# Kernel tuning notes

Hardware: AMD Instinct MI355X
Metric: run time of the kernel (lower is better)

Reference implementation:

```python
import jax, jax.numpy as jnp
import numpy as np

B, C, T = 1024, 64, 275
S = 10            # number of subjects
EMB = 184         # encoder embedding dim
PROJ = 1024       # projector dim
LN_EPS = 1e-5


def setup_inputs() -> dict:
    key = jax.random.key(0)
    ks = jax.random.split(key, 12)
    sc = lambda *shape: 1.0 / np.sqrt(shape[-1] if len(shape) > 1 else 1.0)
    return {
        "eeg": jax.random.normal(ks[0], (B, C, T), dtype=jnp.float32),
        "subject_ids": jax.random.randint(ks[1], (B,), 0, S, dtype=jnp.int64),
        # per-subject Linear(T, T): y = x @ W.T + b
        "subj_W": jax.random.normal(ks[2], (S, T, T), dtype=jnp.float32) / np.sqrt(T),
        "subj_b": jax.random.normal(ks[3], (S, T), dtype=jnp.float32) * 0.02,
        # encoder stub: flatten (C*T) -> Linear -> EMB
        "enc_W": jax.random.normal(ks[4], (C * T, EMB), dtype=jnp.float32) / np.sqrt(C * T),
        "enc_b": jnp.zeros((EMB,), dtype=jnp.float32),
        # projector: Linear(EMB, PROJ) -> ResidualAdd(GELU -> Linear(PROJ, PROJ)) -> LayerNorm
        "W1": jax.random.normal(ks[5], (EMB, PROJ), dtype=jnp.float32) / np.sqrt(EMB),
        "b1": jnp.zeros((PROJ,), dtype=jnp.float32),
        "W2": jax.random.normal(ks[6], (PROJ, PROJ), dtype=jnp.float32) / np.sqrt(PROJ),
        "b2": jnp.zeros((PROJ,), dtype=jnp.float32),
        "gamma": jnp.ones((PROJ,), dtype=jnp.float32),
        "beta": jnp.zeros((PROJ,), dtype=jnp.float32),
    }


def reference(eeg, subject_ids, subj_W, subj_b, enc_W, enc_b, W1, b1, W2, b2, gamma, beta):
    # --- subject-wise alignment: grouped gather -> linear -> scatter ---
    # Vectorized form of the per-subject loop: each row b uses weight subj_W[sid[b]].
    Wg = subj_W[subject_ids]              # [B, T, T]
    bg = subj_b[subject_ids]              # [B, T]
    # torch Linear: y = x @ W.T + b  ->  y[b,c,u] = sum_t eeg[b,c,t] * Wg[b,u,t]
    x = jnp.einsum("bct,but->bcu", eeg, Wg) + bg[:, None, :]   # [B, C, T]

    # --- encoder stub (SpatioTemporalCNN placeholder): flatten + linear ---
    h = x.reshape(x.shape[0], -1) @ enc_W + enc_b              # [B, EMB]

    # --- MLPProjector ---
    h = h @ W1 + b1                                            # [B, PROJ]
    r = jax.nn.gelu(h, approximate=False) @ W2 + b2            # dropout is identity at eval
    h = h + r
    # LayerNorm over last dim
    mu = jnp.mean(h, axis=-1, keepdims=True)
    var = jnp.mean(jnp.square(h - mu), axis=-1, keepdims=True)
    out = (h - mu) * jax.lax.rsqrt(var + LN_EPS) * gamma + beta
    return out
```

## Files before the change

kernel.cpp:

```cpp
#include <hip/hip_runtime.h>
#include <hip/hip_bf16.h>
#include <math.h>

#define B_N    1024
#define C_N    64
#define T_N    275
#define S_N    10
#define EMB_N  184
#define PROJ_N 1024
#define CT_N   (C_N * T_N)
#define TP     288
#define KP2    (C_N * TP)
#define EMBP   192
#define KZ2    16
#define KC2    (KP2 / KZ2)
#define KZ5    2
#define GMAX   264

#define SEC_W   0
#define SEC_E   810
#define SEC_1   1002
#define SEC_2   1050
#define SEC_G   1306
#define SEC_N   1307

typedef unsigned short u16;
typedef __attribute__((ext_vector_type(8))) short short8;
typedef __attribute__((ext_vector_type(4))) short short4v;
typedef __attribute__((ext_vector_type(4))) float f32x4;

#define MFMA16(a,b,c) __builtin_amdgcn_mfma_f32_16x16x32_bf16(a, b, c, 0, 0, 0)

__device__ __forceinline__ u16 f2bf(float f) {
    __hip_bfloat16 h = __float2bfloat16(f);
    return *reinterpret_cast<u16*>(&h);
}
__device__ __forceinline__ float gelu_exact(float v) {
    return 0.5f * v * (1.0f + erff(v * 0.70710678118654752f));
}
__device__ __forceinline__ void gload16(const void* g, void* lds) {
    __builtin_amdgcn_global_load_lds(
        (const __attribute__((address_space(1))) void*)g,
        (__attribute__((address_space(3))) void*)lds, 16, 0, 0);
}

__global__ __launch_bounds__(256) void p_all(
    const int* __restrict__ sid, const float* __restrict__ W,
    const float* __restrict__ encW, const float* __restrict__ W1,
    const float* __restrict__ W2, const float* __restrict__ subj_b,
    u16* __restrict__ Wb, u16* __restrict__ eT, u16* __restrict__ w1t,
    u16* __restrict__ w2t, int* __restrict__ bsq, float* __restrict__ sbp)
{
    __shared__ char smem[16640];
    const int blk = blockIdx.x;
    const int tid = threadIdx.x;

    if (blk < SEC_E) {
        int idx4 = blk * 256 + tid;
        if (idx4 >= S_N * TP * TP / 4) return;
        int o = idx4 * 4;
        int row = o / TP, t = o - row * TP;
        int s = row / TP, u = row - s * TP;
        short4v pk;
        #pragma unroll
        for (int e = 0; e < 4; ++e) {
            float v = (u < T_N && t + e < T_N)
                ? W[((size_t)s * T_N + u) * T_N + t + e] : 0.f;
            pk[e] = (short)f2bf(v);
        }
        *reinterpret_cast<short4v*>(Wb + o) = pk;
        return;
    }
    if (blk < SEC_1) {
        float (*tile)[65] = (float(*)[65])smem;
        int local = blk - SEC_E;
        const int c = local / 3;
        const int n0 = (local % 3) * 64;
        for (int u0 = 0; u0 < TP; u0 += 64) {
            int wlen = (TP - u0 < 64) ? (TP - u0) : 64;
            __syncthreads();
            for (int l = tid; l < 4096; l += 256) {
                int i = l >> 6, j = l & 63;
                int u = u0 + i, n = n0 + j;
                float v = 0.f;
                if (u < T_N && n < EMB_N)
                    v = encW[((size_t)c * T_N + u) * EMB_N + n];
                tile[i][j] = v;
            }
            __syncthreads();
            for (int l = tid; l < 4096; l += 256) {
                int j = l >> 6, i = l & 63;
                if (i < wlen)
                    eT[(size_t)(n0 + j) * KP2 + (size_t)c * TP + u0 + i] =
                        f2bf(tile[i][j]);
            }
        }
        return;
    }
    if (blk < SEC_2) {
        float (*tile)[65] = (float(*)[65])smem;
        int local = blk - SEC_1;
        const int k0 = (local % 3) * 64, n0 = (local / 3) * 64;
        for (int l = tid; l < 4096; l += 256) {
            int i = l >> 6, j = l & 63;
            float v = (k0 + i < EMB_N) ? W1[(size_t)(k0 + i) * PROJ_N + n0 + j] : 0.f;
            tile[i][j] = v;
        }
        __syncthreads();
        for (int l = tid; l < 4096; l += 256) {
            int j = l >> 6, i = l & 63;
            w1t[(size_t)(n0 + j) * EMBP + k0 + i] = f2bf(tile[i][j]);
        }
        return;
    }
    if (blk < SEC_G) {
        float (*tile)[65] = (float(*)[65])smem;
        int local = blk - SEC_2;
        const int k0 = (local % 16) * 64, n0 = (local / 16) * 64;
        for (int l = tid; l < 4096; l += 256) {
            int i = l >> 6, j = l & 63;
            tile[i][j] = W2[(size_t)(k0 + i) * PROJ_N + n0 + j];
        }
        __syncthreads();
        for (int l = tid; l < 4096; l += 256) {
            int j = l >> 6, i = l & 63;
            w2t[(size_t)(n0 + j) * PROJ_N + k0 + i] = f2bf(tile[i][j]);
        }
        return;
    }
    {
        for (int i = tid; i < S_N * TP; i += 256) {
            int s = i / TP, u = i - s * TP;
            sbp[i] = (u < T_N) ? subj_b[s * T_N + u] : 0.f;
        }
        int* sgrp = (int*)smem;
        int* C    = (int*)(smem + 4096);
        int* tot  = (int*)(smem + 4096 + 640);
        for (int i = tid; i < 1024; i += 256) sgrp[i] = sid[i];
        for (int i = tid; i < 4 * GMAX; i += 256) bsq[i] = -1;
        __syncthreads();
        const int w4 = tid >> 6, lane = tid & 63;
        #pragma unroll
        for (int j = 0; j < 4; ++j) {
            int chunk = w4 * 4 + j;
            int sb = sgrp[chunk * 64 + lane];
            int myc = 0;
            for (int s = 0; s < S_N; ++s) {
                unsigned long long m = __ballot(sb == s);
                if (lane == s) myc = (int)__popcll(m);
            }
            if (lane < S_N) C[chunk * S_N + lane] = myc;
        }
        __syncthreads();
        if (tid < S_N) {
            int a = 0;
            for (int w2 = 0; w2 < 16; ++w2) a += C[w2 * S_N + tid];
            tot[tid] = a;
        }
        __syncthreads();
        #pragma unroll
        for (int rep = 0; rep < 4; ++rep) {
            int b = tid + rep * 256;
            int s = sgrp[b];
            int off = 0;
            for (int s2 = 0; s2 < S_N; ++s2)
                if (s2 < s) off += (tot[s2] + 3) & ~3;
            int chunk = b >> 6;
            int rank = 0;
            for (int w2 = 0; w2 < 16; ++w2)
                if (w2 < chunk) rank += C[w2 * S_N + s];
            for (int i = chunk * 64; i < b; ++i) rank += (sgrp[i] == s) ? 1 : 0;
            bsq[off + rank] = b;
        }
    }
}

__global__ __launch_bounds__(512) void k1h(
    const float* __restrict__ eeg, const int* __restrict__ sid,
    const u16* __restrict__ Wb, const float* __restrict__ sbp,
    const int* __restrict__ bsq, u16* __restrict__ xb)
{
    __shared__ __align__(16) u16 Ws[2][TP * 32];
    __shared__ __align__(16) u16 Es[2][128 * 40];
    const int g = blockIdx.x;
    const int b0 = bsq[g * 4];
    if (b0 < 0) return;
    const int ch = blockIdx.y;
    const int s = sid[b0];
    const int tid = threadIdx.x;
    const int w = tid >> 6, lane = tid & 63;
    const int bi = w >> 1, uh = w & 1;
    const int lrow = lane & 15, lk = lane >> 4;
    const int b = bsq[g * 4 + bi];
    const u16* Wr = Wb + (size_t)s * TP * TP;

    const int srow = tid >> 2;
    const int quarter = tid & 3;
    const int bt = srow >> 5, cl = srow & 31;
    int bstage = bsq[g * 4 + bt]; if (bstage < 0) bstage = b0;
    const float* esrc = eeg + (size_t)bstage * CT_N + (ch * 32 + cl) * T_N;

    #define K1_WSTAGE(st, ks)                                                  \
        for (int l = tid; l < TP * 4; l += 512) {                              \
            int u_ = l >> 2, q_ = l & 3;                                       \
            gload16(Wr + (size_t)u_ * TP + (ks) * 32 + ((q_ ^ ((u_ >> 1) & 3)) << 3), \
                    &Ws[st][l * 8]);                                           \
        }
    #define K1_ELOAD(ks, v)                                                    \
        {   int t0_ = (ks) * 32 + quarter * 8;                                 \
            if ((ks) < 8) {                                                    \
                _Pragma("unroll")                                              \
                for (int e = 0; e < 8; ++e) v[e] = esrc[t0_ + e];              \
            } else {                                                           \
                _Pragma("unroll")                                              \
                for (int e = 0; e < 8; ++e)                                    \
                    v[e] = (t0_ + e < T_N) ? esrc[t0_ + e] : 0.f;              \
            }                                                                  \
        }
    #define K1_EWRITE(st, v)                                                   \
        {   short8 pk_;                                                        \
            _Pragma("unroll")                                                  \
            for (int e = 0; e < 8; ++e) pk_[e] = (short)f2bf(v[e]);            \
            *reinterpret_cast<short8*>(&Es[st][srow * 40 + quarter * 8]) = pk_;\
        }

    f32x4 acc[9][2] = {};
    float ev[8], evn[8];

    K1_WSTAGE(0, 0);
    K1_ELOAD(0, ev);
    K1_EWRITE(0, ev);
    __syncthreads();

    for (int ks = 0; ks < 9; ++ks) {
        const int st = ks & 1;
        if (ks < 8) {
            K1_WSTAGE(st ^ 1, ks + 1);
            K1_ELOAD(ks + 1, evn);
        }
        short8 ef[2];
        #pragma unroll
        for (int cf = 0; cf < 2; ++cf)
            ef[cf] = *reinterpret_cast<const short8*>(
                &Es[st][(bi * 32 + cf * 16 + lrow) * 40 + lk * 8]);
        #pragma unroll
        for (int uf = 0; uf < 9; ++uf) {
            int u = uh * 144 + uf * 16 + lrow;
            int chunk = u * 4 + (lk ^ ((u >> 1) & 3));
            short8 av = *reinterpret_cast<const short8*>(&Ws[st][chunk * 8]);
            acc[uf][0] = MFMA16(av, ef[0], acc[uf][0]);
            acc[uf][1] = MFMA16(av, ef[1], acc[uf][1]);
        }
        if (ks < 8) K1_EWRITE(st ^ 1, evn);
        __syncthreads();
    }

    if (b < 0) return;
    u16* xrow = xb + (size_t)b * KP2 + (size_t)(ch * 32) * TP;
    #pragma unroll
    for (int uf = 0; uf < 9; ++uf) {
        int ub = uh * 144 + uf * 16 + 4 * lk;
        float4 b4 = *reinterpret_cast<const float4*>(sbp + s * TP + ub);
        float bias[4] = { b4.x, b4.y, b4.z, b4.w };
        #pragma unroll
        for (int cf = 0; cf < 2; ++cf) {
            int c = cf * 16 + lrow;
            short4v pk;
            #pragma unroll
            for (int r = 0; r < 4; ++r)
                pk[r] = (ub + r < T_N) ? (short)f2bf(acc[uf][cf][r] + bias[r])
                                       : (short)0;
            *reinterpret_cast<short4v*>(xrow + (size_t)c * TP + ub) = pk;
        }
    }
    #undef K1_WSTAGE
    #undef K1_ELOAD
    #undef K1_EWRITE
}

__global__ __launch_bounds__(256) void k2_mfma(
    const u16* __restrict__ xb, const u16* __restrict__ eT,
    float* __restrict__ part)
{
    __shared__ __align__(16) u16 Ab[2][64 * 64];
    const int m0 = blockIdx.x * 64;
    const int kz = blockIdx.y;
    const int kbase = kz * KC2;
    const int tid = threadIdx.x;
    const int w = tid >> 6, lane = tid & 63;
    const int lrow = lane & 15, lk = lane >> 4;

    #define K2_STAGE(st, step)                                                 \
        _Pragma("unroll")                                                      \
        for (int p = 0; p < 2; ++p) {                                          \
            int l = tid + p * 256;                                             \
            int r_ = l >> 3, q_ = l & 7;                                       \
            gload16(xb + (size_t)(m0 + r_) * KP2 + kbase + (step) * 64 +       \
                        ((q_ ^ (r_ & 7)) << 3),                                \
                    &Ab[st][l * 8]);                                           \
        }
    #define K2_BLOAD(step, dst)                                                \
        _Pragma("unroll")                                                      \
        for (int ct = 0; ct < 3; ++ct)                                         \
            _Pragma("unroll")                                                  \
            for (int ki = 0; ki < 2; ++ki)                                     \
                dst[ct][ki] = *reinterpret_cast<const short8*>(                \
                    eT + (size_t)(48 * w + 16 * ct + lrow) * KP2 + kbase +     \
                    (step) * 64 + ki * 32 + 8 * lk);

    f32x4 acc[4][3] = {};
    short8 bf[3][2], bn[3][2];

    K2_STAGE(0, 0);
    K2_BLOAD(0, bf);
    __syncthreads();

    for (int step = 0; step < 18; ++step) {
        const int st = step & 1;
        if (step < 17) {
            K2_STAGE(st ^ 1, step + 1);
            K2_BLOAD(step + 1, bn);
        }
        #pragma unroll
        for (int ki = 0; ki < 2; ++ki)
            #pragma unroll
            for (int rt = 0; rt < 4; ++rt) {
                int m = 16 * rt + lrow;
                int chunk = m * 8 + ((4 * ki + lk) ^ (m & 7));
                short8 af = *reinterpret_cast<const short8*>(&Ab[st][chunk * 8]);
                #pragma unroll
                for (int ct = 0; ct < 3; ++ct)
                    acc[rt][ct] = MFMA16(af, bf[ct][ki], acc[rt][ct]);
            }
        __syncthreads();
        #pragma unroll
        for (int ct = 0; ct < 3; ++ct)
            #pragma unroll
            for (int ki = 0; ki < 2; ++ki) bf[ct][ki] = bn[ct][ki];
    }

    #pragma unroll
    for (int rt = 0; rt < 4; ++rt)
        #pragma unroll
        for (int ct = 0; ct < 3; ++ct) {
            int n = 48 * w + 16 * ct + lrow;
            #pragma unroll
            for (int r = 0; r < 4; ++r) {
                int m = m0 + 16 * rt + 4 * lk + r;
                part[((size_t)kz * B_N + m) * EMBP + n] = acc[rt][ct][r];
            }
        }
    #undef K2_STAGE
    #undef K2_BLOAD
}

__global__ __launch_bounds__(256) void k3_reduce(
    const float* __restrict__ part, const float* __restrict__ enc_b,
    u16* __restrict__ hb)
{
    int idx = blockIdx.x * 256 + threadIdx.x;
    if (idx >= B_N * EMBP) return;
    int n = idx % EMBP;
    float s = 0.f;
    if (n < EMB_N) {
        s = enc_b[n];
        #pragma unroll
        for (int z = 0; z < KZ2; ++z)
            s += part[(size_t)z * B_N * EMBP + idx];
    }
    hb[idx] = f2bf(s);
}

__global__ __launch_bounds__(256) void k4_mfma(
    const u16* __restrict__ hb, const u16* __restrict__ w1t,
    const float* __restrict__ b1, float* __restrict__ h1, u16* __restrict__ g)
{
    __shared__ __align__(16) u16 Ab[64 * EMBP];
    __shared__ __align__(16) u16 Bb[64 * EMBP];
    const int m0 = blockIdx.x * 64, n0 = blockIdx.y * 64;
    const int tid = threadIdx.x;
    const int w = tid >> 6, lane = tid & 63;
    const int wr = w >> 1, wc = w & 1;
    const int lrow = lane & 15, lk = lane >> 4;

    #pragma unroll
    for (int i = 0; i < 6; ++i) {
        int L = tid + i * 256;
        int row = L / 24, qp = L % 24;
        int ql = qp ^ (row & 7);
        gload16(hb  + (size_t)(m0 + row) * EMBP + ql * 8, &Ab[(size_t)L * 8]);
        gload16(w1t + (size_t)(n0 + row) * EMBP + ql * 8, &Bb[(size_t)L * 8]);
    }
    __syncthreads();

    f32x4 acc[2][2] = {};
    #pragma unroll
    for (int ks = 0; ks < 6; ++ks) {
        #pragma unroll
        for (int rt = 0; rt < 2; ++rt) {
            int c = 32 * wr + 16 * rt + lrow;
            short8 af = *reinterpret_cast<const short8*>(
                &Ab[c * EMBP + (((4 * ks + lk) ^ (c & 7)) * 8)]);
            #pragma unroll
            for (int ct = 0; ct < 2; ++ct) {
                int nl = 32 * wc + 16 * ct + lrow;
                short8 bfv = *reinterpret_cast<const short8*>(
                    &Bb[nl * EMBP + (((4 * ks + lk) ^ (nl & 7)) * 8)]);
                acc[rt][ct] = MFMA16(af, bfv, acc[rt][ct]);
            }
        }
    }
    #pragma unroll
    for (int rt = 0; rt < 2; ++rt)
        #pragma unroll
        for (int ct = 0; ct < 2; ++ct) {
            int n = n0 + 32 * wc + 16 * ct + lrow;
            #pragma unroll
            for (int r = 0; r < 4; ++r) {
                int m = m0 + 32 * wr + 16 * rt + 4 * lk + r;
                float v = acc[rt][ct][r] + b1[n];
                size_t o = (size_t)m * PROJ_N + n;
                h1[o] = v;
                g[o] = f2bf(gelu_exact(v));
            }
        }
}

__global__ __launch_bounds__(256) void k5_mfma(
    const u16* __restrict__ g, const u16* __restrict__ w2t,
    float* __restrict__ part2)
{
    __shared__ __align__(16) u16 Ab[2][64 * 64];
    __shared__ __align__(16) u16 Bb[2][64 * 64];
    const int m0 = blockIdx.x * 64, n0 = blockIdx.y * 64;
    const int kz = blockIdx.z;
    const int kbase = kz * (PROJ_N / KZ5);
    const int tid = threadIdx.x;
    const int w = tid >> 6, lane = tid & 63;
    const int wr = w >> 1, wc = w & 1;
    const int lrow = lane & 15, lk = lane >> 4;

    const int r0 = tid >> 3, q0 = tid & 7;
    const int r1 = (tid + 256) >> 3;
    const u16* a0 = g + (size_t)(m0 + r0) * PROJ_N + (q0 ^ (r0 & 7)) * 8;
    const u16* a1 = g + (size_t)(m0 + r1) * PROJ_N + (q0 ^ (r1 & 7)) * 8;
    const u16* b0 = w2t + (size_t)(n0 + r0) * PROJ_N + (q0 ^ (r0 & 7)) * 8;
    const u16* b1p = w2t + (size_t)(n0 + r1) * PROJ_N + (q0 ^ (r1 & 7)) * 8;

    f32x4 acc[2][2] = {};
    int buf = 0;
    gload16(a0 + kbase, &Ab[0][(size_t)(w * 64) * 8]);
    gload16(a1 + kbase, &Ab[0][(size_t)(w * 64 + 256) * 8]);
    gload16(b0 + kbase, &Bb[0][(size_t)(w * 64) * 8]);
    gload16(b1p + kbase, &Bb[0][(size_t)(w * 64 + 256) * 8]);
    __syncthreads();

    for (int step = 0; step < 8; ++step) {
        if (step < 7) {
            int k0 = kbase + (step + 1) * 64;
            gload16(a0 + k0, &Ab[buf ^ 1][(size_t)(w * 64) * 8]);
            gload16(a1 + k0, &Ab[buf ^ 1][(size_t)(w * 64 + 256) * 8]);
            gload16(b0 + k0, &Bb[buf ^ 1][(size_t)(w * 64) * 8]);
            gload16(b1p + k0, &Bb[buf ^ 1][(size_t)(w * 64 + 256) * 8]);
        }
        #pragma unroll
        for (int ki = 0; ki < 2; ++ki) {
            #pragma unroll
            for (int rt = 0; rt < 2; ++rt) {
                int c = 32 * wr + 16 * rt + lrow;
                short8 af = *reinterpret_cast<const short8*>(
                    &Ab[buf][c * 64 + (((lk + 4 * ki) ^ (c & 7)) * 8)]);
                #pragma unroll
                for (int ct = 0; ct < 2; ++ct) {
                    int nl = 32 * wc + 16 * ct + lrow;
                    short8 bfv = *reinterpret_cast<const short8*>(
                        &Bb[buf][nl * 64 + (((lk + 4 * ki) ^ (nl & 7)) * 8)]);
                    acc[rt][ct] = MFMA16(af, bfv, acc[rt][ct]);
                }
            }
        }
        __syncthreads();
        buf ^= 1;
    }
    #pragma unroll
    for (int rt = 0; rt < 2; ++rt)
        #pragma unroll
        for (int ct = 0; ct < 2; ++ct) {
            int n = n0 + 32 * wc + 16 * ct + lrow;
            #pragma unroll
            for (int r = 0; r < 4; ++r) {
                int m = m0 + 32 * wr + 16 * rt + 4 * lk + r;
                part2[(size_t)kz * B_N * PROJ_N + (size_t)m * PROJ_N + n] = acc[rt][ct][r];
            }
        }
}

__global__ __launch_bounds__(256) void k5r_ln(
    const float* __restrict__ part2, const float* __restrict__ h1,
    const float* __restrict__ b2, const float* __restrict__ gamma,
    const float* __restrict__ beta, float* __restrict__ out)
{
    const int m = blockIdx.x;
    const int tid = threadIdx.x;
    const float4* h4 = reinterpret_cast<const float4*>(h1 + (size_t)m * PROJ_N);
    const float4* p0 = reinterpret_cast<const float4*>(part2 + (size_t)m * PROJ_N);
    const float4* p1 = reinterpret_cast<const float4*>(part2 + (size_t)(B_N + m) * PROJ_N);
    const float4* b4 = reinterpret_cast<const float4*>(b2);
    float4 va = h4[tid], vb = p0[tid], vc = p1[tid], vd = b4[tid];
    float v[4] = { va.x + vb.x + vc.x + vd.x, va.y + vb.y + vc.y + vd.y,
                   va.z + vb.z + vc.z + vd.z, va.w + vb.w + vc.w + vd.w };
    float s = 0.f, sq = 0.f;
    #pragma unroll
    for (int i = 0; i < 4; ++i) { s += v[i]; sq += v[i] * v[i]; }
    #pragma unroll
    for (int off = 32; off > 0; off >>= 1) {
        s  += __shfl_down(s, off);
        sq += __shfl_down(sq, off);
    }
    __shared__ float ss[4], ssq[4];
    int wid = tid >> 6, lane = tid & 63;
    if (lane == 0) { ss[wid] = s; ssq[wid] = sq; }
    __syncthreads();
    if (tid == 0) {
        float a = 0.f, bsum = 0.f;
        #pragma unroll
        for (int q = 0; q < 4; ++q) { a += ss[q]; bsum += ssq[q]; }
        ss[0] = a; ssq[0] = bsum;
    }
    __syncthreads();
    float mu  = ss[0] * (1.0f / PROJ_N);
    float var = ssq[0] * (1.0f / PROJ_N) - mu * mu;
    float rs  = rsqrtf(var + 1e-5f);
    const float4 g4 = reinterpret_cast<const float4*>(gamma)[tid];
    const float4 be4 = reinterpret_cast<const float4*>(beta)[tid];
    float gg[4] = { g4.x, g4.y, g4.z, g4.w };
    float bb[4] = { be4.x, be4.y, be4.z, be4.w };
    float4 o4;
    float* op = reinterpret_cast<float*>(&o4);
    #pragma unroll
    for (int i = 0; i < 4; ++i) op[i] = (v[i] - mu) * rs * gg[i] + bb[i];
    reinterpret_cast<float4*>(out + (size_t)m * PROJ_N)[tid] = o4;
}

extern "C" void kernel_launch(void* const* d_in, const int* in_sizes, int n_in,
                              void* d_out, int out_size, void* d_ws, size_t ws_size,
                              hipStream_t stream)
{
    const float* eeg    = (const float*)d_in[0];
    const int*   sid    = (const int*)  d_in[1];
    const float* subj_W = (const float*)d_in[2];
    const float* subj_b = (const float*)d_in[3];
    const float* enc_W  = (const float*)d_in[4];
    const float* enc_b  = (const float*)d_in[5];
    const float* W1     = (const float*)d_in[6];
    const float* b1     = (const float*)d_in[7];
    const float* W2     = (const float*)d_in[8];
    const float* b2     = (const float*)d_in[9];
    const float* gamma  = (const float*)d_in[10];
    const float* beta   = (const float*)d_in[11];
    float* out = (float*)d_out;

    char* w = (char*)d_ws;
    u16*   xb    = (u16*)(w);
    u16*   Wb    = (u16*)(w + 37748736);
    u16*   eT    = (u16*)(w + 39407616);
    u16*   w1t   = (u16*)(w + 46485504);
    u16*   w2t   = (u16*)(w + 46878720);
    u16*   hb    = (u16*)(w + 48975872);
    float* h1    = (float*)(w + 49369088);
    u16*   g     = (u16*)(w + 53563392);
    float* sbp   = (float*)(w + 55660544);
    int*   bsq   = (int*)(w + 55672064);
    float* part  = (float*)(w + 55676288);
    float* part2 = (float*)(w + 68259200);

    p_all<<<dim3(SEC_N), 256, 0, stream>>>(sid, subj_W, enc_W, W1, W2, subj_b,
                                           Wb, eT, w1t, w2t, bsq, sbp);
    k1h  <<<dim3(GMAX, 2), 512, 0, stream>>>(eeg, sid, Wb, sbp, bsq, xb);
    k2_mfma<<<dim3(16, KZ2), 256, 0, stream>>>(xb, eT, part);
    k3_reduce<<<dim3((B_N * EMBP + 255) / 256), 256, 0, stream>>>(part, enc_b, hb);
    k4_mfma<<<dim3(16, 16), 256, 0, stream>>>(hb, w1t, b1, h1, g);
    k5_mfma<<<dim3(16, 16, KZ5), 256, 0, stream>>>(g, w2t, part2);
    k5r_ln <<<dim3(B_N), 256, 0, stream>>>(part2, h1, b2, gamma, beta, out);
}
```

Baseline: 120.8 us.

## Preload whole EEG tile with vectorized loads and split k1 blocks in half

The subject-alignment kernel now loads the full 32-channel by 275-sample EEG slab for two batch rows into shared memory up front, using contiguous float4 loads converted to bf16. This replaces the per-K-step strided scalar loads that were double-buffered. Blocks shrink from 512 to 256 threads and the grid doubles, so each block handles two batch rows instead of four. The trade-off is more shared memory per block, no overlap between the EEG load and compute, and the subject weight slab now being staged twice as often.

```diff
diff --git a/kernel.cpp b/kernel.cpp
--- a/kernel.cpp
+++ b/kernel.cpp
@@ -16,6 +16,7 @@
 #define KC2    (KP2 / KZ2)
 #define KZ5    2
 #define GMAX   264
+#define ESTR   296
 
 #define SEC_W   0
 #define SEC_E   810
@@ -175,74 +176,66 @@
     }
 }
 
-__global__ __launch_bounds__(512) void k1h(
+__global__ __launch_bounds__(256) void k1v(
     const float* __restrict__ eeg, const int* __restrict__ sid,
     const u16* __restrict__ Wb, const float* __restrict__ sbp,
     const int* __restrict__ bsq, u16* __restrict__ xb)
 {
+    __shared__ __align__(16) u16 Es[64 * ESTR];
     __shared__ __align__(16) u16 Ws[2][TP * 32];
-    __shared__ __align__(16) u16 Es[2][128 * 40];
     const int g = blockIdx.x;
     const int b0 = bsq[g * 4];
     if (b0 < 0) return;
-    const int ch = blockIdx.y;
+    const int p = blockIdx.y >> 1, ch = blockIdx.y & 1;
     const int s = sid[b0];
     const int tid = threadIdx.x;
     const int w = tid >> 6, lane = tid & 63;
     const int bi = w >> 1, uh = w & 1;
     const int lrow = lane & 15, lk = lane >> 4;
-    const int b = bsq[g * 4 + bi];
+    const int b = bsq[g * 4 + p * 2 + bi];
     const u16* Wr = Wb + (size_t)s * TP * TP;
 
-    const int srow = tid >> 2;
-    const int quarter = tid & 3;
-    const int bt = srow >> 5, cl = srow & 31;
-    int bstage = bsq[g * 4 + bt]; if (bstage < 0) bstage = b0;
-    const float* esrc = eeg + (size_t)bstage * CT_N + (ch * 32 + cl) * T_N;
-
     #define K1_WSTAGE(st, ks)                                                  \
-        for (int l = tid; l < TP * 4; l += 512) {                              \
+        for (int l = tid; l < TP * 4; l += 256) {                              \
             int u_ = l >> 2, q_ = l & 3;                                       \
             gload16(Wr + (size_t)u_ * TP + (ks) * 32 + ((q_ ^ ((u_ >> 1) & 3)) << 3), \
                     &Ws[st][l * 8]);                                           \
         }
-    #define K1_ELOAD(ks, v)                                                    \
-        {   int t0_ = (ks) * 32 + quarter * 8;                                 \
-            if ((ks) < 8) {                                                    \
-                _Pragma("unroll")                                              \
-                for (int e = 0; e < 8; ++e) v[e] = esrc[t0_ + e];              \
-            } else {                                                           \
-                _Pragma("unroll")                                              \
-                for (int e = 0; e < 8; ++e)                                    \
-                    v[e] = (t0_ + e < T_N) ? esrc[t0_ + e] : 0.f;              \
-            }                                                                  \
-        }
-    #define K1_EWRITE(st, v)                                                   \
-        {   short8 pk_;                                                        \
-            _Pragma("unroll")                                                  \
-            for (int e = 0; e < 8; ++e) pk_[e] = (short)f2bf(v[e]);            \
-            *reinterpret_cast<short8*>(&Es[st][srow * 40 + quarter * 8]) = pk_;\
-        }
+
+    K1_WSTAGE(0, 0);
+    #pragma unroll
+    for (int reg = 0; reg < 2; ++reg) {
+        int bstage = bsq[g * 4 + p * 2 + reg]; if (bstage < 0) bstage = b0;
+        const float4* src4 = reinterpret_cast<const float4*>(
+            eeg + (size_t)bstage * CT_N + ch * 32 * T_N);
+        for (int l = tid; l < (32 * T_N) / 4; l += 256) {
+            float4 v = src4[l];
+            float vv[4] = { v.x, v.y, v.z, v.w };
+            int o = l * 4;
+            int r = o / T_N, c0 = o - r * T_N;
+            #pragma unroll
+            for (int e = 0; e < 4; ++e) {
+                int r2 = r, c2 = c0 + e;
+                if (c2 >= T_N) { r2++; c2 -= T_N; }
+                Es[(reg * 32 + r2) * ESTR + c2] = f2bf(vv[e]);
+            }
+        }
+    }
+    for (int l = tid; l < 64 * (TP - T_N); l += 256) {
+        int r = l / (TP - T_N), c = T_N + (l - r * (TP - T_N));
+        Es[r * ESTR + c] = 0;
+    }
+    __syncthreads();
 
     f32x4 acc[9][2] = {};
-    float ev[8], evn[8];
-
-    K1_WSTAGE(0, 0);
-    K1_ELOAD(0, ev);
-    K1_EWRITE(0, ev);
-    __syncthreads();
-
     for (int ks = 0; ks < 9; ++ks) {
         const int st = ks & 1;
-        if (ks < 8) {
-            K1_WSTAGE(st ^ 1, ks + 1);
-            K1_ELOAD(ks + 1, evn);
-        }
+        if (ks < 8) K1_WSTAGE(st ^ 1, ks + 1);
         short8 ef[2];
         #pragma unroll
         for (int cf = 0; cf < 2; ++cf)
             ef[cf] = *reinterpret_cast<const short8*>(
-                &Es[st][(bi * 32 + cf * 16 + lrow) * 40 + lk * 8]);
+                &Es[(bi * 32 + cf * 16 + lrow) * ESTR + ks * 32 + lk * 8]);
         #pragma unroll
         for (int uf = 0; uf < 9; ++uf) {
             int u = uh * 144 + uf * 16 + lrow;
@@ -251,7 +244,6 @@
             acc[uf][0] = MFMA16(av, ef[0], acc[uf][0]);
             acc[uf][1] = MFMA16(av, ef[1], acc[uf][1]);
         }
-        if (ks < 8) K1_EWRITE(st ^ 1, evn);
         __syncthreads();
     }
 
@@ -274,8 +266,6 @@
         }
     }
     #undef K1_WSTAGE
-    #undef K1_ELOAD
-    #undef K1_EWRITE
 }
 
 __global__ __launch_bounds__(256) void k2_mfma(
@@ -576,7 +566,7 @@
 
     p_all<<<dim3(SEC_N), 256, 0, stream>>>(sid, subj_W, enc_W, W1, W2, subj_b,
                                            Wb, eT, w1t, w2t, bsq, sbp);
-    k1h  <<<dim3(GMAX, 2), 512, 0, stream>>>(eeg, sid, Wb, sbp, bsq, xb);
+    k1v  <<<dim3(GMAX, 4), 256, 0, stream>>>(eeg, sid, Wb, sbp, bsq, xb);
     k2_mfma<<<dim3(16, KZ2), 256, 0, stream>>>(xb, eT, part);
     k3_reduce<<<dim3((B_N * EMBP + 255) / 256), 256, 0, stream>>>(part, enc_b, hb);
     k4_mfma<<<dim3(16, 16), 256, 0, stream>>>(hb, w1t, b1, h1, g);
```

Result: slower. 130.9 us (+8.4%).

## Triple-buffer subject weight tiles in k1 with counted vmcnt waits

Applied to the files above, without the earlier changes.

The per-subject alignment GEMM kernel now keeps three LDS buffers for the weight tiles and prefetches two k-steps ahead, replacing __syncthreads with raw s_barrier plus per-wave vmcnt waits so async global-to-LDS loads can stay in flight across iterations. It also raises wave priority around the MFMA block. This is meant to hide global load latency in k1, at the cost of more LDS per block (possible occupancy loss) and fragile hand-counted vmcnt values.

```diff
diff --git a/kernel.cpp b/kernel.cpp
--- a/kernel.cpp
+++ b/kernel.cpp
@@ -175,12 +175,12 @@
     }
 }
 
-__global__ __launch_bounds__(512) void k1h(
+__global__ __launch_bounds__(512) void k1p(
     const float* __restrict__ eeg, const int* __restrict__ sid,
     const u16* __restrict__ Wb, const float* __restrict__ sbp,
     const int* __restrict__ bsq, u16* __restrict__ xb)
 {
-    __shared__ __align__(16) u16 Ws[2][TP * 32];
+    __shared__ __align__(16) u16 Ws[3][TP * 32];
     __shared__ __align__(16) u16 Es[2][128 * 40];
     const int g = blockIdx.x;
     const int b0 = bsq[g * 4];
@@ -200,11 +200,11 @@
     int bstage = bsq[g * 4 + bt]; if (bstage < 0) bstage = b0;
     const float* esrc = eeg + (size_t)bstage * CT_N + (ch * 32 + cl) * T_N;
 
-    #define K1_WSTAGE(st, ks)                                                  \
+    #define K1_WSTAGE(bufi, ks)                                                \
         for (int l = tid; l < TP * 4; l += 512) {                              \
             int u_ = l >> 2, q_ = l & 3;                                       \
             gload16(Wr + (size_t)u_ * TP + (ks) * 32 + ((q_ ^ ((u_ >> 1) & 3)) << 3), \
-                    &Ws[st][l * 8]);                                           \
+                    &Ws[bufi][l * 8]);                                         \
         }
     #define K1_ELOAD(ks, v)                                                    \
         {   int t0_ = (ks) * 32 + quarter * 8;                                 \
@@ -223,36 +223,45 @@
             for (int e = 0; e < 8; ++e) pk_[e] = (short)f2bf(v[e]);            \
             *reinterpret_cast<short8*>(&Es[st][srow * 40 + quarter * 8]) = pk_;\
         }
+    #define K1_WAITN()                                                         \
+        {   if (w < 2) asm volatile("s_waitcnt vmcnt(3) lgkmcnt(0)" ::: "memory"); \
+            else       asm volatile("s_waitcnt vmcnt(2) lgkmcnt(0)" ::: "memory"); }
 
     f32x4 acc[9][2] = {};
     float ev[8], evn[8];
 
+    K1_ELOAD(0, ev);
     K1_WSTAGE(0, 0);
-    K1_ELOAD(0, ev);
+    K1_WSTAGE(1, 1);
     K1_EWRITE(0, ev);
-    __syncthreads();
+    K1_WAITN();
+    __builtin_amdgcn_s_barrier();
 
     for (int ks = 0; ks < 9; ++ks) {
-        const int st = ks & 1;
-        if (ks < 8) {
-            K1_WSTAGE(st ^ 1, ks + 1);
-            K1_ELOAD(ks + 1, evn);
-        }
+        const int wb = ks % 3, eb = ks & 1;
+        if (ks < 8) K1_ELOAD(ks + 1, evn);
+        if (ks < 7) K1_WSTAGE((ks + 2) % 3, ks + 2);
+
         short8 ef[2];
         #pragma unroll
         for (int cf = 0; cf < 2; ++cf)
             ef[cf] = *reinterpret_cast<const short8*>(
-                &Es[st][(bi * 32 + cf * 16 + lrow) * 40 + lk * 8]);
+                &Es[eb][(bi * 32 + cf * 16 + lrow) * 40 + lk * 8]);
+        __builtin_amdgcn_s_setprio(1);
         #pragma unroll
         for (int uf = 0; uf < 9; ++uf) {
             int u = uh * 144 + uf * 16 + lrow;
             int chunk = u * 4 + (lk ^ ((u >> 1) & 3));
-            short8 av = *reinterpret_cast<const short8*>(&Ws[st][chunk * 8]);
+            short8 av = *reinterpret_cast<const short8*>(&Ws[wb][chunk * 8]);
             acc[uf][0] = MFMA16(av, ef[0], acc[uf][0]);
             acc[uf][1] = MFMA16(av, ef[1], acc[uf][1]);
         }
-        if (ks < 8) K1_EWRITE(st ^ 1, evn);
-        __syncthreads();
+        __builtin_amdgcn_s_setprio(0);
+
+        if (ks < 8) K1_EWRITE(eb ^ 1, evn);
+        if (ks < 7) { K1_WAITN(); }
+        else asm volatile("s_waitcnt vmcnt(0) lgkmcnt(0)" ::: "memory");
+        if (ks < 8) __builtin_amdgcn_s_barrier();
     }
 
     if (b < 0) return;
@@ -276,6 +285,7 @@
     #undef K1_WSTAGE
     #undef K1_ELOAD
     #undef K1_EWRITE
+    #undef K1_WAITN
 }
 
 __global__ __launch_bounds__(256) void k2_mfma(
@@ -576,7 +586,7 @@
 
     p_all<<<dim3(SEC_N), 256, 0, stream>>>(sid, subj_W, enc_W, W1, W2, subj_b,
                                            Wb, eT, w1t, w2t, bsq, sbp);
-    k1h  <<<dim3(GMAX, 2), 512, 0, stream>>>(eeg, sid, Wb, sbp, bsq, xb);
+    k1p  <<<dim3(GMAX, 2), 512, 0, stream>>>(eeg, sid, Wb, sbp, bsq, xb);
     k2_mfma<<<dim3(16, KZ2), 256, 0, stream>>>(xb, eT, part);
     k3_reduce<<<dim3((B_N * EMBP + 255) / 256), 256, 0, stream>>>(part, enc_b, hb);
     k4_mfma<<<dim3(16, 16), 256, 0, stream>>>(hb, w1t, b1, h1, g);
```

Result: no change. 118.4 us, median of 3 (-1.9%).
